# Kernel tuning notes

Hardware: AMD Instinct MI355X
Metric: run time of the kernel (lower is better)

The kernel has to match this reference:

```python
import jax, jax.numpy as jnp
import numpy as np

B, MAXLEN, F, D = 1024, 200, 64, 64
NEG_PAD = -2.0**32 + 1.0  # tf.ones_like(a) * (-2**32 + 1)


def setup_inputs() -> dict:
    key = jax.random.key(0)
    ks = jax.random.split(key, 9)
    return {
        "q": jax.random.normal(ks[0], (B, F, D), jnp.float32),
        "k": jax.random.normal(ks[1], (B, MAXLEN, D), jnp.float32),
        "v": jax.random.normal(ks[2], (B, MAXLEN, D), jnp.float32),
        "kes_length": jax.random.randint(ks[3], (B, 1), 0, MAXLEN, dtype=jnp.int32),
        "field_strengths": jax.random.normal(ks[4], (F, 1), jnp.float32) * 0.05,
        "bias": jax.random.normal(ks[5], (1,), jnp.float32) * 0.05,
        "W_query": jax.random.normal(ks[6], (D, D), jnp.float32) * 0.05,
        "W_key": jax.random.normal(ks[7], (D, D), jnp.float32) * 0.05,
        "W_value": jax.random.normal(ks[8], (D, D), jnp.float32) * 0.05,
    }


def reference(q, k, v, kes_length, field_strengths, bias, W_query, W_key, W_value):
    # is_keys_diff=True branch: project q/k, and v comes from projected k
    qp = jnp.einsum('bfd,de->bfe', q, W_query)   # [B,F,D]
    vp = jnp.einsum('btd,de->bte', k, W_value)   # [B,T,D]
    kp = jnp.einsum('btd,de->bte', k, W_key)     # [B,T,D]

    # Original: tile q->[B,T,F,D], k->[B,T,F,D], a=q*k*fs, sum over F (+bias),
    # then sum over D.  Fused: score[b,t] = sum_d (sum_f qp[b,f,d]*fs[f]) * kp[b,t,d]
    # and the +bias inside [B,T,D] then sum over D contributes bias*D.
    fs = field_strengths[:, 0]                   # [F]
    qw = jnp.einsum('bfd,f->bd', qp, fs)         # field-weighted query, [B,D]
    score = jnp.einsum('bd,btd->bt', qw, kp) + bias[0] * D  # [B,T]

    a = jax.nn.sigmoid(score)
    mask = jnp.arange(MAXLEN)[None, :] < kes_length[:, :1]  # sequence_mask, [B,T]
    a = jnp.where(mask, a, jnp.float32(NEG_PAD))
    a = a / jnp.sqrt(jnp.float32(D))             # / emb_dim**0.5 (after masking, as in source)
    a = jax.nn.softmax(a, axis=-1)               # weight_softmax=True

    out = jnp.einsum('bt,btd->bd', a, vp)        # [B,1,T] @ [B,T,D]
    return out[:, None, :]                       # [B,1,D]
```

## Files before the change

### kernel.cpp

```cpp
#include <hip/hip_runtime.h>
#include <math.h>


namespace {
constexpr int MAXLEN = 200;
constexpr int FF     = 64;
constexpr int DD     = 64;
constexpr int TILE   = 64;
constexpr int ROWP   = 65;

__global__ __launch_bounds__(256, 8)
void auto_attn_kernel(const float* __restrict__ q,
                      const float* __restrict__ k,
                      const int*   __restrict__ kes_length,
                      const float* __restrict__ fs,
                      const float* __restrict__ bias,
                      const float* __restrict__ Wq,
                      const float* __restrict__ Wk,
                      const float* __restrict__ Wv,
                      float*       __restrict__ out)
{
    __shared__ float kt[TILE * ROWP];
    __shared__ float red[256];
    __shared__ float qbar[DD];
    __shared__ float qw[DD];
    __shared__ float qk[DD];
    __shared__ float kbar[DD];
    __shared__ float sw[TILE];
    __shared__ float sS[4];

    const int tid = threadIdx.x;
    const int b   = blockIdx.x;
    const int d   = tid & 63;
    const int grp = tid >> 6;

    const float* qb = q + (size_t)b * FF * DD;
    const float* kb = k + (size_t)b * MAXLEN * DD;
    const int len   = kes_length[b];

    float acc = 0.f;
    for (int i = 0; i < 16; ++i) {
        const int f = grp * 16 + i;
        acc += fs[f] * qb[f * 64 + d];
    }
    red[tid] = acc;
    __syncthreads();
    if (tid < 64) qbar[tid] = red[tid] + red[tid + 64] + red[tid + 128] + red[tid + 192];
    __syncthreads();

    acc = 0.f;
    for (int i = 0; i < 16; ++i) {
        const int dd = grp * 16 + i;
        acc += qbar[dd] * Wq[dd * 64 + d];
    }
    red[tid] = acc;
    __syncthreads();
    if (tid < 64) qw[tid] = red[tid] + red[tid + 64] + red[tid + 128] + red[tid + 192];
    __syncthreads();

    for (int j = 0; j < 4; ++j) {
        const int base = (tid + 256 * j) * 4;
        const float4 w4 = *(const float4*)(Wk + base);
        const int row = base >> 6, col = base & 63;
        float* p = &kt[row * ROWP + col];
        p[0] = w4.x; p[1] = w4.y; p[2] = w4.z; p[3] = w4.w;
    }
    __syncthreads();
    acc = 0.f;
    for (int i = 0; i < 16; ++i) {
        const int e = grp * 16 + i;
        acc += kt[d * ROWP + e] * qw[e];
    }
    red[tid] = acc;
    __syncthreads();
    if (tid < 64) qk[tid] = red[tid] + red[tid + 64] + red[tid + 128] + red[tid + 192];
    __syncthreads();

    const float bscale = bias[0] * 64.0f;

    float kaccr = 0.f;
    float Sr    = 0.f;
    const int tok = tid >> 2;
    const int dq  = (tid & 3) << 4;

    for (int tile = 0; tile < 4; ++tile) {
        const int t0   = tile * TILE;
        const int tlen = min(TILE, MAXLEN - t0);
        for (int j = tid; j < tlen * 16; j += 256) {
            const int base = j * 4;
            const float4 kv = *(const float4*)(kb + t0 * 64 + base);
            const int row = base >> 6, col = base & 63;
            float* p = &kt[row * ROWP + col];
            p[0] = kv.x; p[1] = kv.y; p[2] = kv.z; p[3] = kv.w;
        }
        __syncthreads();
        if (tok < tlen) {
            float s = 0.f;
            const float* rowp = &kt[tok * ROWP + dq];
            for (int i = 0; i < 16; ++i) s += rowp[i] * qk[dq + i];
            s += __shfl_xor(s, 1);
            s += __shfl_xor(s, 2);
            s += bscale;
            const int t = t0 + tok;
            float w;
            if (len == 0)      w = 1.0f;
            else if (t < len) { const float sig = 1.0f / (1.0f + expf(-s));
                                w = expf(sig * 0.125f); }
            else               w = 0.0f;
            if ((tid & 3) == 0) sw[tok] = w;
        }
        __syncthreads();
        const int nt = min(16, tlen - grp * 16);
        for (int i = 0; i < nt; ++i) {
            const int tl = grp * 16 + i;
            const float w = sw[tl];
            kaccr += w * kt[tl * ROWP + d];
            Sr    += w;
        }
        __syncthreads();
    }

    red[tid] = kaccr;
    if (d == 0) sS[grp] = Sr;
    __syncthreads();
    if (tid < 64) {
        const float kv = red[tid] + red[tid + 64] + red[tid + 128] + red[tid + 192];
        const float S  = sS[0] + sS[1] + sS[2] + sS[3];
        kbar[tid] = kv / S;
    }
    __syncthreads();
    acc = 0.f;
    for (int i = 0; i < 16; ++i) {
        const int dd = grp * 16 + i;
        acc += kbar[dd] * Wv[dd * 64 + d];
    }
    red[tid] = acc;
    __syncthreads();
    if (tid < 64) out[(size_t)b * 64 + tid] = red[tid] + red[tid + 64] + red[tid + 128] + red[tid + 192];
}
}

extern "C" void kernel_launch(void* const* d_in, const int* in_sizes, int n_in,
                              void* d_out, int out_size, void* d_ws, size_t ws_size,
                              hipStream_t stream) {
    const float* q    = (const float*)d_in[0];
    const float* k    = (const float*)d_in[1];
    const int*   kes  = (const int*)  d_in[3];
    const float* fs   = (const float*)d_in[4];
    const float* bias = (const float*)d_in[5];
    const float* Wq   = (const float*)d_in[6];
    const float* Wk   = (const float*)d_in[7];
    const float* Wv   = (const float*)d_in[8];
    float* out = (float*)d_out;

    auto_attn_kernel<<<dim3(1024), dim3(256), 0, stream>>>(q, k, kes, fs, bias, Wq, Wk, Wv, out);
}
```

Measured before the change: 140.6 us.

## Prefetch whole K row block into LDS asynchronously, overlapping with query projection

At kernel entry, each block issues direct global-to-LDS loads (global_load_lds) for the entire 200x64 key slice, so these transfers overlap with the q/Wq/Wk projection phase instead of running as four tiled load-compute steps. Each of 200 threads then computes one token score with a rotated index to avoid bank conflicts, and the weighted sum runs in a single pass with fewer barriers. The Wk staging through LDS is replaced by direct global reads, and fast __expf is used. The trade-off is about 52KB of LDS per block with launch bounds lowered to 4 blocks, which reduces occupancy. It also relies on the async LDS loads having completed by the first barrier.

```diff
diff --git a/kernel.cpp b/kernel.cpp
--- a/kernel.cpp
+++ b/kernel.cpp
@@ -4,12 +4,16 @@
 
 namespace {
 constexpr int MAXLEN = 200;
-constexpr int FF     = 64;
 constexpr int DD     = 64;
-constexpr int TILE   = 64;
-constexpr int ROWP   = 65;
 
-__global__ __launch_bounds__(256, 8)
+__device__ __forceinline__ void load_lds16(const float* g, float* l) {
+    __builtin_amdgcn_global_load_lds(
+        (const __attribute__((address_space(1))) void*)g,
+        (__attribute__((address_space(3))) void*)l,
+        16, 0, 0);
+}
+
+__global__ __launch_bounds__(256, 4)
 void auto_attn_kernel(const float* __restrict__ q,
                       const float* __restrict__ k,
                       const int*   __restrict__ kes_length,
@@ -20,123 +24,105 @@
                       const float* __restrict__ Wv,
                       float*       __restrict__ out)
 {
-    __shared__ float kt[TILE * ROWP];
+    __shared__ float kt[MAXLEN * DD];
     __shared__ float red[256];
-    __shared__ float qbar[DD];
-    __shared__ float qw[DD];
-    __shared__ float qk[DD];
-    __shared__ float kbar[DD];
-    __shared__ float sw[TILE];
+    __shared__ float vec[DD];
+    __shared__ float qks[DD];
+    __shared__ float sw[MAXLEN];
     __shared__ float sS[4];
 
-    const int tid = threadIdx.x;
-    const int b   = blockIdx.x;
-    const int d   = tid & 63;
-    const int grp = tid >> 6;
+    const int tid  = threadIdx.x;
+    const int b    = blockIdx.x;
+    const int lane = tid & 63;
+    const int wave = tid >> 6;
 
-    const float* qb = q + (size_t)b * FF * DD;
-    const float* kb = k + (size_t)b * MAXLEN * DD;
-    const int len   = kes_length[b];
+    const float* kb = k + (size_t)b * (MAXLEN * DD);
+    const float* qb = q + (size_t)b * (DD * DD);
+
+    for (int j = wave; j < 50; j += 4)
+        load_lds16(kb + j * 256 + lane * 4, &kt[j * 256]);
+
+    const int len = kes_length[b];
 
     float acc = 0.f;
+    #pragma unroll
     for (int i = 0; i < 16; ++i) {
-        const int f = grp * 16 + i;
-        acc += fs[f] * qb[f * 64 + d];
+        const int f = wave * 16 + i;
+        acc += fs[f] * qb[f * 64 + lane];
     }
     red[tid] = acc;
     __syncthreads();
-    if (tid < 64) qbar[tid] = red[tid] + red[tid + 64] + red[tid + 128] + red[tid + 192];
+    if (tid < 64) vec[tid] = red[tid] + red[tid + 64] + red[tid + 128] + red[tid + 192];
     __syncthreads();
 
     acc = 0.f;
+    #pragma unroll
     for (int i = 0; i < 16; ++i) {
-        const int dd = grp * 16 + i;
-        acc += qbar[dd] * Wq[dd * 64 + d];
+        const int dd = wave * 16 + i;
+        acc += vec[dd] * Wq[dd * 64 + lane];
     }
     red[tid] = acc;
     __syncthreads();
-    if (tid < 64) qw[tid] = red[tid] + red[tid + 64] + red[tid + 128] + red[tid + 192];
+    if (tid < 64) vec[tid] = red[tid] + red[tid + 64] + red[tid + 128] + red[tid + 192];
     __syncthreads();
 
-    for (int j = 0; j < 4; ++j) {
-        const int base = (tid + 256 * j) * 4;
-        const float4 w4 = *(const float4*)(Wk + base);
-        const int row = base >> 6, col = base & 63;
-        float* p = &kt[row * ROWP + col];
-        p[0] = w4.x; p[1] = w4.y; p[2] = w4.z; p[3] = w4.w;
-    }
-    __syncthreads();
     acc = 0.f;
+    #pragma unroll
     for (int i = 0; i < 16; ++i) {
-        const int e = grp * 16 + i;
-        acc += kt[d * ROWP + e] * qw[e];
+        const int e = wave * 16 + i;
+        acc += Wk[lane * 64 + e] * vec[e];
     }
     red[tid] = acc;
     __syncthreads();
-    if (tid < 64) qk[tid] = red[tid] + red[tid + 64] + red[tid + 128] + red[tid + 192];
+    if (tid < 64) qks[tid] = red[tid] + red[tid + 64] + red[tid + 128] + red[tid + 192];
     __syncthreads();
 
     const float bscale = bias[0] * 64.0f;
+    const int t = tid;
+    if (t < MAXLEN) {
+        float s = 0.f;
+        #pragma unroll
+        for (int i = 0; i < 64; ++i) {
+            const int idx = (i + lane) & 63;
+            s += kt[t * 64 + idx] * qks[idx];
+        }
+        s += bscale;
+        float w;
+        if (len == 0)      w = 1.0f;
+        else if (t < len) { const float sig = 1.0f / (1.0f + __expf(-s));
+                            w = __expf(sig * 0.125f); }
+        else               w = 0.0f;
+        sw[t] = w;
+    }
+    __syncthreads();
 
-    float kaccr = 0.f;
-    float Sr    = 0.f;
-    const int tok = tid >> 2;
-    const int dq  = (tid & 3) << 4;
-
-    for (int tile = 0; tile < 4; ++tile) {
-        const int t0   = tile * TILE;
-        const int tlen = min(TILE, MAXLEN - t0);
-        for (int j = tid; j < tlen * 16; j += 256) {
-            const int base = j * 4;
-            const float4 kv = *(const float4*)(kb + t0 * 64 + base);
-            const int row = base >> 6, col = base & 63;
-            float* p = &kt[row * ROWP + col];
-            p[0] = kv.x; p[1] = kv.y; p[2] = kv.z; p[3] = kv.w;
-        }
-        __syncthreads();
-        if (tok < tlen) {
-            float s = 0.f;
-            const float* rowp = &kt[tok * ROWP + dq];
-            for (int i = 0; i < 16; ++i) s += rowp[i] * qk[dq + i];
-            s += __shfl_xor(s, 1);
-            s += __shfl_xor(s, 2);
-            s += bscale;
-            const int t = t0 + tok;
-            float w;
-            if (len == 0)      w = 1.0f;
-            else if (t < len) { const float sig = 1.0f / (1.0f + expf(-s));
-                                w = expf(sig * 0.125f); }
-            else               w = 0.0f;
-            if ((tid & 3) == 0) sw[tok] = w;
-        }
-        __syncthreads();
-        const int nt = min(16, tlen - grp * 16);
-        for (int i = 0; i < nt; ++i) {
-            const int tl = grp * 16 + i;
-            const float w = sw[tl];
-            kaccr += w * kt[tl * ROWP + d];
-            Sr    += w;
-        }
-        __syncthreads();
+    float kacc = 0.f, Sr = 0.f;
+    #pragma unroll 10
+    for (int i = 0; i < 50; ++i) {
+        const int t2 = wave * 50 + i;
+        const float w = sw[t2];
+        kacc += w * kt[t2 * 64 + lane];
+        Sr   += w;
     }
-
-    red[tid] = kaccr;
-    if (d == 0) sS[grp] = Sr;
+    red[tid] = kacc;
+    if (lane == 0) sS[wave] = Sr;
     __syncthreads();
     if (tid < 64) {
-        const float kv = red[tid] + red[tid + 64] + red[tid + 128] + red[tid + 192];
-        const float S  = sS[0] + sS[1] + sS[2] + sS[3];
-        kbar[tid] = kv / S;
+        const float S = sS[0] + sS[1] + sS[2] + sS[3];
+        vec[tid] = (red[tid] + red[tid + 64] + red[tid + 128] + red[tid + 192]) / S;
     }
     __syncthreads();
+
     acc = 0.f;
+    #pragma unroll
     for (int i = 0; i < 16; ++i) {
-        const int dd = grp * 16 + i;
-        acc += kbar[dd] * Wv[dd * 64 + d];
+        const int dd = wave * 16 + i;
+        acc += vec[dd] * Wv[dd * 64 + lane];
     }
     red[tid] = acc;
     __syncthreads();
-    if (tid < 64) out[(size_t)b * 64 + tid] = red[tid] + red[tid + 64] + red[tid + 128] + red[tid + 192];
+    if (tid < 64)
+        out[(size_t)b * 64 + tid] = red[tid] + red[tid + 64] + red[tid + 128] + red[tid + 192];
 }
 }
 
```

Result: no change. 142.4 us (+1.3%).
